# Performance work log

Measured on AMD Instinct MI355X. Metric: run time of the kernel, lower is better.

Reference implementation:

```python
import jax, jax.numpy as jnp
import numpy as np

H = 12        # num_attention_heads
D = 768       # hidden_size
DH = D // H   # attention_size per head (64)
B, S = 1, 4096


def setup_inputs() -> dict:
    key = jax.random.key(0)
    ks = jax.random.split(key, 10)
    scale = 0.02
    x = jax.random.normal(ks[0], (B, S, D), dtype=jnp.float32)
    # per-head QKV weights stacked: [H, D, DH]
    wq = jax.random.normal(ks[1], (H, D, DH), dtype=jnp.float32) * scale
    wk = jax.random.normal(ks[2], (H, D, DH), dtype=jnp.float32) * scale
    wv = jax.random.normal(ks[3], (H, D, DH), dtype=jnp.float32) * scale
    bq = jax.random.normal(ks[4], (H, DH), dtype=jnp.float32) * scale
    bk = jax.random.normal(ks[5], (H, DH), dtype=jnp.float32) * scale
    bv = jax.random.normal(ks[6], (H, DH), dtype=jnp.float32) * scale
    wo = jax.random.normal(ks[7], (D, D), dtype=jnp.float32) * scale
    bo = jax.random.normal(ks[8], (D,), dtype=jnp.float32) * scale
    return {"x": x, "wq": wq, "bq": bq, "wk": wk, "bk": bk,
            "wv": wv, "bv": bv, "wo": wo, "bo": bo}


def reference(x, wq, bq, wk, bk, wv, bv, wo, bo):
    # per-head linear projections: [B,S,D] x [H,D,DH] -> [B,H,S,DH]
    q = jnp.einsum('bsd,hde->bhse', x, wq) + bq[None, :, None, :]
    k = jnp.einsum('bsd,hde->bhse', x, wk) + bk[None, :, None, :]
    v = jnp.einsum('bsd,hde->bhse', x, wv) + bv[None, :, None, :]
    # scaled dot-product attention, full NxN probs as in original
    scores = jnp.einsum('bhse,bhte->bhst', q, k) / jnp.sqrt(jnp.float32(DH))
    probs = jax.nn.softmax(scores, axis=-1)          # [B,H,S,S]
    ctx = jnp.einsum('bhst,bhte->bhse', probs, v)    # [B,H,S,DH]
    # concat heads along feature dim (head order = original ModuleList order)
    ctx = jnp.transpose(ctx, (0, 2, 1, 3)).reshape(B, S, H * DH)
    out = ctx @ wo + bo                               # output projection
    return out
```

## Files before the change

### kernel.cpp

```cpp
#include <hip/hip_runtime.h>


using frag8 = __attribute__((ext_vector_type(8))) short;
using facc4 = __attribute__((ext_vector_type(4))) float;
using uint4v = __attribute__((ext_vector_type(4))) unsigned int;

#define LOG2E 1.4426950408889634f
#define THR_LOG2 11.5415603f
#define SWZ16(r, b) ((b) ^ (((r) & 7) << 4))

#if defined(__has_builtin)
#  if __has_builtin(__builtin_amdgcn_exp2f)
#    define EXP2(x) __builtin_amdgcn_exp2f(x)
#  else
#    define EXP2(x) exp2f(x)
#  endif
#else
#  define EXP2(x) exp2f(x)
#endif

__device__ __forceinline__ unsigned short f2bf(float f) {
  unsigned int u = __builtin_bit_cast(unsigned int, f);
  u = (u + 0x7FFFu + ((u >> 16) & 1u)) >> 16;
  return (unsigned short)u;
}
__device__ __forceinline__ float bf2f(unsigned short s) {
  unsigned int u = ((unsigned int)s) << 16;
  return __builtin_bit_cast(float, u);
}
__device__ __forceinline__ unsigned cvt_pk_bf16(float lo, float hi) {
  unsigned r;
  asm("v_cvt_pk_bf16_f32 %0, %1, %2" : "=v"(r) : "v"(lo), "v"(hi));
  return r;
}

__device__ __forceinline__ facc4 mfma_bf16(frag8 a, frag8 b, facc4 c) {
  return __builtin_amdgcn_mfma_f32_16x16x32_bf16(a, b, c, 0, 0, 0);
}

__device__ __forceinline__ void gld_lds16(const void* g, void* l) {
  auto gp = (const __attribute__((address_space(1))) unsigned int*)g;
  auto lp = (__attribute__((address_space(3))) unsigned int*)l;
  __builtin_amdgcn_global_load_lds(gp, lp, 16, 0, 0);
}

__global__ __launch_bounds__(256) void k_cvt_x(const float* __restrict__ in,
                                               unsigned short* __restrict__ out) {
  int i = (blockIdx.x * 256 + threadIdx.x) * 8;
  float4 a = *(const float4*)(in + i);
  float4 b = *(const float4*)(in + i + 4);
  frag8 r;
  r[0] = (short)f2bf(a.x); r[1] = (short)f2bf(a.y);
  r[2] = (short)f2bf(a.z); r[3] = (short)f2bf(a.w);
  r[4] = (short)f2bf(b.x); r[5] = (short)f2bf(b.y);
  r[6] = (short)f2bf(b.z); r[7] = (short)f2bf(b.w);
  *(frag8*)(out + i) = r;
}

__global__ __launch_bounds__(256) void k_prep_w(
    const float* __restrict__ wq, const float* __restrict__ wk,
    const float* __restrict__ wv, const float* __restrict__ wo,
    unsigned short* __restrict__ wqT, unsigned short* __restrict__ wkT,
    unsigned short* __restrict__ wvT, unsigned short* __restrict__ woT) {
  __shared__ unsigned short tile[64][65];
  const int bx = blockIdx.x;
  const float* src; unsigned short* dst;
  int ld_src, ld_dst, r0, c0;
  if (bx < 432) {
    int p = bx / 144, rem = bx % 144;
    int h = rem / 12, dt = rem % 12;
    src = (p == 0 ? wq : (p == 1 ? wk : wv)) + (size_t)h * 768 * 64;
    dst = (p == 0 ? wqT : (p == 1 ? wkT : wvT)) + (size_t)h * 64 * 768;
    ld_src = 64; ld_dst = 768; r0 = dt * 64; c0 = 0;
  } else {
    int t = bx - 432;
    src = wo; dst = woT;
    ld_src = 768; ld_dst = 768;
    r0 = (t / 12) * 64; c0 = (t % 12) * 64;
  }
  const int tid = threadIdx.x;
  const int lr = tid >> 2, lc0 = (tid & 3) * 16;
#pragma unroll
  for (int i = 0; i < 16; ++i)
    tile[lr][lc0 + i] = f2bf(src[(size_t)(r0 + lr) * ld_src + c0 + lc0 + i]);
  __syncthreads();
  const int oc = tid >> 2;
#pragma unroll
  for (int i = 0; i < 16; ++i)
    dst[(size_t)(c0 + oc) * ld_dst + r0 + lc0 + i] = tile[lc0 + i][oc];
}

__global__ __launch_bounds__(256) void k_qkv(
    const unsigned short* __restrict__ xb, const unsigned short* __restrict__ wT,
    const float* __restrict__ bq, const float* __restrict__ bk,
    const float* __restrict__ bv,
    unsigned short* __restrict__ qo, unsigned short* __restrict__ ko,
    unsigned short* __restrict__ vTo) {
  __shared__ __align__(16) unsigned short As[128 * 64];
  __shared__ __align__(16) unsigned short Bs[64 * 64];
  const int sb = blockIdx.x, ph = blockIdx.y;
  const int p = ph / 12, h = ph % 12;
  const int s0 = sb * 128;
  const int tid = threadIdx.x;
  const int w = tid >> 6, l = tid & 63;
  const int lg = l >> 4, li = l & 15;
  const int wm = w >> 1, wn = w & 1;
  const unsigned short* wTb = wT + (size_t)ph * 64 * 768;

  facc4 acc[4][2];
#pragma unroll
  for (int i = 0; i < 4; ++i)
#pragma unroll
    for (int j = 0; j < 2; ++j) acc[i][j] = (facc4){0.f, 0.f, 0.f, 0.f};

  const int rA = tid >> 3;
  const int cbp = (tid & 7) * 16;

  for (int k0 = 0; k0 < 768; k0 += 64) {
#pragma unroll
    for (int i = 0; i < 4; ++i) {
      int r = i * 32 + rA;
      gld_lds16((const char*)(xb + (size_t)(s0 + r) * 768 + k0) + SWZ16(r, cbp),
                (char*)As + i * 4096 + w * 1024);
    }
#pragma unroll
    for (int i = 0; i < 2; ++i) {
      int r = i * 32 + rA;
      gld_lds16((const char*)(wTb + (size_t)r * 768 + k0) + SWZ16(r, cbp),
                (char*)Bs + i * 4096 + w * 1024);
    }
    __syncthreads();
#pragma unroll
    for (int kk = 0; kk < 2; ++kk) {
      const int cbl = kk * 64 + lg * 16;
      frag8 a[4], b[2];
#pragma unroll
      for (int mf = 0; mf < 4; ++mf) {
        int r = wm * 64 + mf * 16 + li;
        a[mf] = *(const frag8*)((const char*)As + r * 128 + SWZ16(r, cbl));
      }
#pragma unroll
      for (int nf = 0; nf < 2; ++nf) {
        int r = wn * 32 + nf * 16 + li;
        b[nf] = *(const frag8*)((const char*)Bs + r * 128 + SWZ16(r, cbl));
      }
#pragma unroll
      for (int mf = 0; mf < 4; ++mf)
#pragma unroll
        for (int nf = 0; nf < 2; ++nf)
          acc[mf][nf] = mfma_bf16(a[mf], b[nf], acc[mf][nf]);
    }
    __syncthreads();
  }

  const float* bias = (p == 0 ? bq : (p == 1 ? bk : bv)) + h * 64;
  const float scale = (p == 0) ? 0.125f * LOG2E : 1.0f;
  float bvv[2];
#pragma unroll
  for (int nf = 0; nf < 2; ++nf) bvv[nf] = bias[wn * 32 + nf * 16 + li];
#pragma unroll
  for (int mf = 0; mf < 4; ++mf)
#pragma unroll
    for (int nf = 0; nf < 2; ++nf) {
      int e = wn * 32 + nf * 16 + li;
#pragma unroll
      for (int j = 0; j < 4; ++j) {
        int s = s0 + wm * 64 + mf * 16 + lg * 4 + j;
        unsigned short bf = f2bf((acc[mf][nf][j] + bvv[nf]) * scale);
        if (p == 0)      qo[((size_t)h * 4096 + s) * 64 + e] = bf;
        else if (p == 1) ko[((size_t)h * 4096 + s) * 64 + e] = bf;
        else             vTo[((size_t)h * 64 + e) * 4096 + s] = bf;
      }
    }
}

__global__ __launch_bounds__(512) void k_attn(
    const unsigned short* __restrict__ q, const unsigned short* __restrict__ k,
    const unsigned short* __restrict__ vT,
    unsigned short* __restrict__ oP, float* __restrict__ mlP) {
  __shared__ __align__(16) char Kb[2][8192];
  __shared__ __align__(16) char Vb[2][8192];
  const int bid = blockIdx.x;
  const int part = blockIdx.y;
  const int h = bid >> 5, qb = bid & 31;
  const int s0 = qb * 128;
  const int tid = threadIdx.x;
  const int w = tid >> 6, l = tid & 63;
  const int lg = l >> 4, li = l & 15;
  const unsigned short* Kh = k + (size_t)h * 4096 * 64;
  const unsigned short* Vh = vT + (size_t)h * 64 * 4096;

  const int rS = tid >> 3;
  const int bS = (tid & 7) * 16;
  const int sbS = SWZ16(rS, bS);

  const unsigned short* qrow = q + ((size_t)h * 4096 + s0 + w * 16 + li) * 64;
  frag8 qf0 = *(const frag8*)(qrow + lg * 8);
  frag8 qf1 = *(const frag8*)(qrow + 32 + lg * 8);

  frag8 onesf;
#pragma unroll
  for (int i = 0; i < 8; ++i) onesf[i] = (short)0x3F80;

  const int a_ = li >> 2, b_ = li & 3;
  const int r_base = 8 * a_ + b_;
  int kOff[4][2], vOff[4][2];
#pragma unroll
  for (int cn = 0; cn < 4; ++cn) {
    int r = r_base + 4 * ((cn & 1) ^ (a_ & 1)) + 32 * (cn >> 1);
    kOff[cn][0] = r * 128 + SWZ16(r, lg * 16);
    kOff[cn][1] = r * 128 + SWZ16(r, 64 + lg * 16);
  }
#pragma unroll
  for (int nf = 0; nf < 4; ++nf) {
    int rv = nf * 16 + li;
    vOff[nf][0] = rv * 128 + SWZ16(rv, lg * 16);
    vOff[nf][1] = rv * 128 + SWZ16(rv, 64 + lg * 16);
  }
  const char* KbC = (const char*)Kb;
  const char* VbC = (const char*)Vb;

  float m = -1e30f;
  facc4 acc[4];
  facc4 accl = (facc4){0.f, 0.f, 0.f, 0.f};
#pragma unroll
  for (int nf = 0; nf < 4; ++nf) acc[nf] = (facc4){0.f, 0.f, 0.f, 0.f};

  const int kb0 = part * 2048;

  gld_lds16((const char*)(Kh + (size_t)(kb0 + rS) * 64) + sbS, (char*)Kb + w * 1024);
  gld_lds16((const char*)(Vh + (size_t)rS * 4096 + kb0) + sbS, (char*)Vb + w * 1024);
  const char* KgN = (const char*)(Kh + (size_t)(kb0 + 64 + rS) * 64) + sbS;
  const char* VgN = (const char*)(Vh + (size_t)rS * 4096 + kb0 + 64) + sbS;
  __syncthreads();

#define ATTN_STEP(BUFB, KT)                                                   \
  {                                                                           \
    if ((KT) < 31) {                                                          \
      gld_lds16(KgN, (char*)Kb + ((BUFB) ^ 8192) + w * 1024);                 \
      gld_lds16(VgN, (char*)Vb + ((BUFB) ^ 8192) + w * 1024);                 \
      KgN += 8192; VgN += 128;                                                \
    }                                                                         \
    facc4 sf[4];                                                              \
    __builtin_amdgcn_s_setprio(1);                                            \
    _Pragma("unroll")                                                         \
    for (int cn = 0; cn < 4; ++cn) {                                          \
      frag8 a0 = *(const frag8*)(KbC + (BUFB) + kOff[cn][0]);                 \
      frag8 a1 = *(const frag8*)(KbC + (BUFB) + kOff[cn][1]);                 \
      facc4 s = (facc4){0.f, 0.f, 0.f, 0.f};                                  \
      s = mfma_bf16(a0, qf0, s);                                              \
      s = mfma_bf16(a1, qf1, s);                                              \
      sf[cn] = s;                                                             \
    }                                                                         \
    __builtin_amdgcn_s_setprio(0);                                            \
    if (lg & 1) {                                                             \
      facc4 t_ = sf[0]; sf[0] = sf[1]; sf[1] = t_;                            \
      t_ = sf[2]; sf[2] = sf[3]; sf[3] = t_;                                  \
    }                                                                         \
    float t = fmaxf(fmaxf(sf[0][0], sf[0][1]), sf[0][2]);                     \
    t = fmaxf(fmaxf(t, sf[0][3]), sf[1][0]);                                  \
    t = fmaxf(fmaxf(t, sf[1][1]), sf[1][2]);                                  \
    t = fmaxf(fmaxf(t, sf[1][3]), sf[2][0]);                                  \
    t = fmaxf(fmaxf(t, sf[2][1]), sf[2][2]);                                  \
    t = fmaxf(fmaxf(t, sf[2][3]), sf[3][0]);                                  \
    t = fmaxf(fmaxf(t, sf[3][1]), sf[3][2]);                                  \
    float tmax = fmaxf(t, sf[3][3]);                                          \
    tmax = fmaxf(tmax, __shfl_xor(tmax, 16));                                 \
    tmax = fmaxf(tmax, __shfl_xor(tmax, 32));                                 \
    if (__any(tmax > m + THR_LOG2)) {                                         \
      float mn = fmaxf(m, tmax);                                              \
      float corr = EXP2(m - mn);                                              \
      m = mn;                                                                 \
      _Pragma("unroll")                                                       \
      for (int j = 0; j < 4; ++j) {                                           \
        float cj = __shfl(corr, (l & 48) | (4 * lg + j));                     \
        accl[j] *= cj;                                                        \
        _Pragma("unroll")                                                     \
        for (int nf = 0; nf < 4; ++nf) acc[nf][j] *= cj;                      \
      }                                                                       \
    }                                                                         \
    float pv[4][4];                                                           \
    _Pragma("unroll")                                                         \
    for (int cn = 0; cn < 4; ++cn)                                            \
      _Pragma("unroll")                                                       \
      for (int j = 0; j < 4; ++j)                                             \
        pv[cn][j] = EXP2(sf[cn][j] - m);                                      \
    uint4v u0, u1;                                                            \
    u0[0] = cvt_pk_bf16(pv[0][0], pv[0][1]);                                  \
    u0[1] = cvt_pk_bf16(pv[0][2], pv[0][3]);                                  \
    u0[2] = cvt_pk_bf16(pv[1][0], pv[1][1]);                                  \
    u0[3] = cvt_pk_bf16(pv[1][2], pv[1][3]);                                  \
    u1[0] = cvt_pk_bf16(pv[2][0], pv[2][1]);                                  \
    u1[1] = cvt_pk_bf16(pv[2][2], pv[2][3]);                                  \
    u1[2] = cvt_pk_bf16(pv[3][0], pv[3][1]);                                  \
    u1[3] = cvt_pk_bf16(pv[3][2], pv[3][3]);                                  \
    frag8 pa0 = __builtin_bit_cast(frag8, u0);                                \
    frag8 pa1 = __builtin_bit_cast(frag8, u1);                                \
    __builtin_amdgcn_s_setprio(1);                                            \
    accl = mfma_bf16(pa0, onesf, accl);                                       \
    accl = mfma_bf16(pa1, onesf, accl);                                       \
    _Pragma("unroll")                                                         \
    for (int nf = 0; nf < 4; ++nf) {                                          \
      frag8 vb0 = *(const frag8*)(VbC + (BUFB) + vOff[nf][0]);                \
      frag8 vb1 = *(const frag8*)(VbC + (BUFB) + vOff[nf][1]);                \
      acc[nf] = mfma_bf16(pa0, vb0, acc[nf]);                                 \
      acc[nf] = mfma_bf16(pa1, vb1, acc[nf]);                                 \
    }                                                                         \
    __builtin_amdgcn_s_setprio(0);                                            \
    __syncthreads();                                                          \
  }

  for (int t2 = 0; t2 < 16; ++t2) {
    ATTN_STEP(0, 2 * t2)
    ATTN_STEP(8192, 2 * t2 + 1)
  }
#undef ATTN_STEP

  const size_t base = ((size_t)(part * 12 + h) * 4096 + s0 + w * 16);
#pragma unroll
  for (int nf = 0; nf < 4; ++nf)
#pragma unroll
    for (int j = 0; j < 4; ++j)
      oP[(base + lg * 4 + j) * 64 + nf * 16 + li] = f2bf(acc[nf][j] / accl[j]);
  if (lg == 0)
    mlP[(base + li) * 2 + 0] = m;
  if (li == 0) {
#pragma unroll
    for (int j = 0; j < 4; ++j)
      mlP[(base + lg * 4 + j) * 2 + 1] = accl[j];
  }
}

__global__ __launch_bounds__(256) void k_combine(
    const unsigned short* __restrict__ oP, const float* __restrict__ mlP,
    unsigned short* __restrict__ ctx) {
  const int tid = threadIdx.x;
  const int rg = blockIdx.x * 4 + (tid >> 6);
  const int e = tid & 63;
  const int h = rg >> 12, s = rg & 4095;
  const size_t r0 = (size_t)h * 4096 + s;
  const size_t r1 = (size_t)(12 + h) * 4096 + s;
  float m0 = mlP[r0 * 2], l0 = mlP[r0 * 2 + 1];
  float m1 = mlP[r1 * 2], l1 = mlP[r1 * 2 + 1];
  float M = fmaxf(m0, m1);
  float w0 = l0 * EXP2(m0 - M);
  float w1 = l1 * EXP2(m1 - M);
  float inv = 1.f / (w0 + w1);
  float o = (w0 * bf2f(oP[r0 * 64 + e]) + w1 * bf2f(oP[r1 * 64 + e])) * inv;
  ctx[(size_t)s * 768 + h * 64 + e] = f2bf(o);
}

__global__ __launch_bounds__(256) void k_proj(
    const unsigned short* __restrict__ ctx, const unsigned short* __restrict__ woT,
    const float* __restrict__ bo, float* __restrict__ out) {
  __shared__ __align__(16) unsigned short As[64 * 64];
  __shared__ __align__(16) unsigned short Bs[64 * 64];
  const int s0 = blockIdx.x * 64, j0 = blockIdx.y * 64;
  const int tid = threadIdx.x;
  const int w = tid >> 6, l = tid & 63;
  const int lg = l >> 4, li = l & 15;
  const int wm = w >> 1, wn = w & 1;
  facc4 acc[2][2];
#pragma unroll
  for (int i = 0; i < 2; ++i)
#pragma unroll
    for (int j = 0; j < 2; ++j) acc[i][j] = (facc4){0.f, 0.f, 0.f, 0.f};

  const int rA = tid >> 3;
  const int cbp = (tid & 7) * 16;

  for (int k0 = 0; k0 < 768; k0 += 64) {
#pragma unroll
    for (int i = 0; i < 2; ++i) {
      int r = i * 32 + rA;
      gld_lds16((const char*)(ctx + (size_t)(s0 + r) * 768 + k0) + SWZ16(r, cbp),
                (char*)As + i * 4096 + w * 1024);
      gld_lds16((const char*)(woT + (size_t)(j0 + r) * 768 + k0) + SWZ16(r, cbp),
                (char*)Bs + i * 4096 + w * 1024);
    }
    __syncthreads();
#pragma unroll
    for (int kk = 0; kk < 2; ++kk) {
      const int cbl = kk * 64 + lg * 16;
      frag8 a[2], b[2];
#pragma unroll
      for (int mf = 0; mf < 2; ++mf) {
        int r = wm * 32 + mf * 16 + li;
        a[mf] = *(const frag8*)((const char*)As + r * 128 + SWZ16(r, cbl));
      }
#pragma unroll
      for (int nf = 0; nf < 2; ++nf) {
        int r = wn * 32 + nf * 16 + li;
        b[nf] = *(const frag8*)((const char*)Bs + r * 128 + SWZ16(r, cbl));
      }
#pragma unroll
      for (int mf = 0; mf < 2; ++mf)
#pragma unroll
        for (int nf = 0; nf < 2; ++nf)
          acc[mf][nf] = mfma_bf16(a[mf], b[nf], acc[mf][nf]);
    }
    __syncthreads();
  }
#pragma unroll
  for (int nf = 0; nf < 2; ++nf) {
    int jc = j0 + wn * 32 + nf * 16 + li;
    float bb = bo[jc];
#pragma unroll
    for (int mf = 0; mf < 2; ++mf)
#pragma unroll
      for (int j = 0; j < 4; ++j) {
        int s = s0 + wm * 32 + mf * 16 + lg * 4 + j;
        out[(size_t)s * 768 + jc] = acc[mf][nf][j] + bb;
      }
  }
}

extern "C" void kernel_launch(void* const* d_in, const int* in_sizes, int n_in,
                              void* d_out, int out_size, void* d_ws, size_t ws_size,
                              hipStream_t stream) {
  const float* x  = (const float*)d_in[0];
  const float* wq = (const float*)d_in[1];
  const float* bq = (const float*)d_in[2];
  const float* wk = (const float*)d_in[3];
  const float* bk = (const float*)d_in[4];
  const float* wv = (const float*)d_in[5];
  const float* bv = (const float*)d_in[6];
  const float* wo = (const float*)d_in[7];
  const float* bo = (const float*)d_in[8];
  float* out = (float*)d_out;

  char* ws = (char*)d_ws;
  unsigned short* xb  = (unsigned short*)(ws);
  unsigned short* wT  = (unsigned short*)(ws + 6291456);
  unsigned short* woT = (unsigned short*)(ws + 9830400);
  unsigned short* qd  = (unsigned short*)(ws + 11010048);
  unsigned short* kd  = (unsigned short*)(ws + 17301504);
  unsigned short* vTd = (unsigned short*)(ws + 23592960);
  unsigned short* ctx = (unsigned short*)(ws + 29884416);
  unsigned short* oP  = (unsigned short*)(ws + 36175872);
  float*          mlP = (float*)(ws + 48758784);

  k_cvt_x<<<1536, 256, 0, stream>>>(x, xb);
  k_prep_w<<<576, 256, 0, stream>>>(wq, wk, wv, wo,
                                    wT, wT + 589824, wT + 1179648, woT);
  k_qkv<<<dim3(32, 36), 256, 0, stream>>>(xb, wT, bq, bk, bv, qd, kd, vTd);
  k_attn<<<dim3(384, 2), 512, 0, stream>>>(qd, kd, vTd, oP, mlP);
  k_combine<<<12288, 256, 0, stream>>>(oP, mlP, ctx);
  k_proj<<<dim3(64, 12), 256, 0, stream>>>(ctx, woT, bo, out);
}
```

Measured before the change: 137.1 us.

## Triple-buffer attention K/V loads and widen QKV GEMM tile to 128 columns

The attention kernel moves from double to triple buffering of K/V tiles in LDS. It replaces __syncthreads with an explicit s_waitcnt vmcnt(2) plus s_barrier, so the next tile's loads stay in flight across the barrier. The QKV projection kernel now computes 128x128 tiles covering two heads per block, halving the grid and reusing each loaded x tile across twice as many output columns. The costs are higher LDS use per block in both kernels and more accumulator registers in QKV, which may reduce occupancy.

```diff
diff --git a/kernel.cpp b/kernel.cpp
--- a/kernel.cpp
+++ b/kernel.cpp
@@ -97,21 +97,19 @@
     unsigned short* __restrict__ qo, unsigned short* __restrict__ ko,
     unsigned short* __restrict__ vTo) {
   __shared__ __align__(16) unsigned short As[128 * 64];
-  __shared__ __align__(16) unsigned short Bs[64 * 64];
-  const int sb = blockIdx.x, ph = blockIdx.y;
-  const int p = ph / 12, h = ph % 12;
-  const int s0 = sb * 128;
+  __shared__ __align__(16) unsigned short Bs[128 * 64];
+  const int sb = blockIdx.x, nb = blockIdx.y;
+  const int s0 = sb * 128, c0 = nb * 128;
   const int tid = threadIdx.x;
   const int w = tid >> 6, l = tid & 63;
   const int lg = l >> 4, li = l & 15;
   const int wm = w >> 1, wn = w & 1;
-  const unsigned short* wTb = wT + (size_t)ph * 64 * 768;
-
-  facc4 acc[4][2];
+
+  facc4 acc[4][4];
 #pragma unroll
   for (int i = 0; i < 4; ++i)
 #pragma unroll
-    for (int j = 0; j < 2; ++j) acc[i][j] = (facc4){0.f, 0.f, 0.f, 0.f};
+    for (int j = 0; j < 4; ++j) acc[i][j] = (facc4){0.f, 0.f, 0.f, 0.f};
 
   const int rA = tid >> 3;
   const int cbp = (tid & 7) * 16;
@@ -122,64 +120,60 @@
       int r = i * 32 + rA;
       gld_lds16((const char*)(xb + (size_t)(s0 + r) * 768 + k0) + SWZ16(r, cbp),
                 (char*)As + i * 4096 + w * 1024);
-    }
-#pragma unroll
-    for (int i = 0; i < 2; ++i) {
-      int r = i * 32 + rA;
-      gld_lds16((const char*)(wTb + (size_t)r * 768 + k0) + SWZ16(r, cbp),
+      gld_lds16((const char*)(wT + (size_t)(c0 + r) * 768 + k0) + SWZ16(r, cbp),
                 (char*)Bs + i * 4096 + w * 1024);
     }
     __syncthreads();
 #pragma unroll
     for (int kk = 0; kk < 2; ++kk) {
       const int cbl = kk * 64 + lg * 16;
-      frag8 a[4], b[2];
+      frag8 a[4], b[4];
 #pragma unroll
       for (int mf = 0; mf < 4; ++mf) {
         int r = wm * 64 + mf * 16 + li;
         a[mf] = *(const frag8*)((const char*)As + r * 128 + SWZ16(r, cbl));
       }
 #pragma unroll
-      for (int nf = 0; nf < 2; ++nf) {
-        int r = wn * 32 + nf * 16 + li;
+      for (int nf = 0; nf < 4; ++nf) {
+        int r = wn * 64 + nf * 16 + li;
         b[nf] = *(const frag8*)((const char*)Bs + r * 128 + SWZ16(r, cbl));
       }
 #pragma unroll
       for (int mf = 0; mf < 4; ++mf)
 #pragma unroll
-        for (int nf = 0; nf < 2; ++nf)
+        for (int nf = 0; nf < 4; ++nf)
           acc[mf][nf] = mfma_bf16(a[mf], b[nf], acc[mf][nf]);
     }
     __syncthreads();
   }
 
+  const int ph = nb * 2 + wn;
+  const int p = ph / 12, h = ph % 12;
   const float* bias = (p == 0 ? bq : (p == 1 ? bk : bv)) + h * 64;
   const float scale = (p == 0) ? 0.125f * LOG2E : 1.0f;
-  float bvv[2];
-#pragma unroll
-  for (int nf = 0; nf < 2; ++nf) bvv[nf] = bias[wn * 32 + nf * 16 + li];
-#pragma unroll
-  for (int mf = 0; mf < 4; ++mf)
-#pragma unroll
-    for (int nf = 0; nf < 2; ++nf) {
-      int e = wn * 32 + nf * 16 + li;
+#pragma unroll
+  for (int nf = 0; nf < 4; ++nf) {
+    int e = nf * 16 + li;
+    float bvv = bias[e];
+#pragma unroll
+    for (int mf = 0; mf < 4; ++mf)
 #pragma unroll
       for (int j = 0; j < 4; ++j) {
         int s = s0 + wm * 64 + mf * 16 + lg * 4 + j;
-        unsigned short bf = f2bf((acc[mf][nf][j] + bvv[nf]) * scale);
+        unsigned short bf = f2bf((acc[mf][nf][j] + bvv) * scale);
         if (p == 0)      qo[((size_t)h * 4096 + s) * 64 + e] = bf;
         else if (p == 1) ko[((size_t)h * 4096 + s) * 64 + e] = bf;
         else             vTo[((size_t)h * 64 + e) * 4096 + s] = bf;
       }
-    }
+  }
 }
 
 __global__ __launch_bounds__(512) void k_attn(
     const unsigned short* __restrict__ q, const unsigned short* __restrict__ k,
     const unsigned short* __restrict__ vT,
     unsigned short* __restrict__ oP, float* __restrict__ mlP) {
-  __shared__ __align__(16) char Kb[2][8192];
-  __shared__ __align__(16) char Vb[2][8192];
+  __shared__ __align__(16) char Kb[3][8192];
+  __shared__ __align__(16) char Vb[3][8192];
   const int bid = blockIdx.x;
   const int part = blockIdx.y;
   const int h = bid >> 5, qb = bid & 31;
@@ -228,25 +222,32 @@
 
   const int kb0 = part * 2048;
 
-  gld_lds16((const char*)(Kh + (size_t)(kb0 + rS) * 64) + sbS, (char*)Kb + w * 1024);
-  gld_lds16((const char*)(Vh + (size_t)rS * 4096 + kb0) + sbS, (char*)Vb + w * 1024);
-  const char* KgN = (const char*)(Kh + (size_t)(kb0 + 64 + rS) * 64) + sbS;
-  const char* VgN = (const char*)(Vh + (size_t)rS * 4096 + kb0 + 64) + sbS;
-  __syncthreads();
-
-#define ATTN_STEP(BUFB, KT)                                                   \
+  gld_lds16((const char*)(Kh + (size_t)(kb0 + rS) * 64) + sbS,
+            (char*)Kb + w * 1024);
+  gld_lds16((const char*)(Vh + (size_t)rS * 4096 + kb0) + sbS,
+            (char*)Vb + w * 1024);
+  gld_lds16((const char*)(Kh + (size_t)(kb0 + 64 + rS) * 64) + sbS,
+            (char*)Kb + 8192 + w * 1024);
+  gld_lds16((const char*)(Vh + (size_t)rS * 4096 + kb0 + 64) + sbS,
+            (char*)Vb + 8192 + w * 1024);
+  const char* KgN = (const char*)(Kh + (size_t)(kb0 + 128 + rS) * 64) + sbS;
+  const char* VgN = (const char*)(Vh + (size_t)rS * 4096 + kb0 + 128) + sbS;
+  asm volatile("s_waitcnt vmcnt(2)" ::: "memory");
+  __builtin_amdgcn_s_barrier();
+
+#define ATTN_STEP(CURB, NXTB, DO_ISSUE, DO_SYNC, VMSTR)                       \
   {                                                                           \
-    if ((KT) < 31) {                                                          \
-      gld_lds16(KgN, (char*)Kb + ((BUFB) ^ 8192) + w * 1024);                 \
-      gld_lds16(VgN, (char*)Vb + ((BUFB) ^ 8192) + w * 1024);                 \
+    if (DO_ISSUE) {                                                           \
+      gld_lds16(KgN, (char*)Kb + (NXTB) + w * 1024);                          \
+      gld_lds16(VgN, (char*)Vb + (NXTB) + w * 1024);                          \
       KgN += 8192; VgN += 128;                                                \
     }                                                                         \
     facc4 sf[4];                                                              \
     __builtin_amdgcn_s_setprio(1);                                            \
     _Pragma("unroll")                                                         \
     for (int cn = 0; cn < 4; ++cn) {                                          \
-      frag8 a0 = *(const frag8*)(KbC + (BUFB) + kOff[cn][0]);                 \
-      frag8 a1 = *(const frag8*)(KbC + (BUFB) + kOff[cn][1]);                 \
+      frag8 a0 = *(const frag8*)(KbC + (CURB) + kOff[cn][0]);                 \
+      frag8 a1 = *(const frag8*)(KbC + (CURB) + kOff[cn][1]);                 \
       facc4 s = (facc4){0.f, 0.f, 0.f, 0.f};                                  \
       s = mfma_bf16(a0, qf0, s);                                              \
       s = mfma_bf16(a1, qf1, s);                                              \
@@ -301,19 +302,25 @@
     accl = mfma_bf16(pa1, onesf, accl);                                       \
     _Pragma("unroll")                                                         \
     for (int nf = 0; nf < 4; ++nf) {                                          \
-      frag8 vb0 = *(const frag8*)(VbC + (BUFB) + vOff[nf][0]);                \
-      frag8 vb1 = *(const frag8*)(VbC + (BUFB) + vOff[nf][1]);                \
+      frag8 vb0 = *(const frag8*)(VbC + (CURB) + vOff[nf][0]);                \
+      frag8 vb1 = *(const frag8*)(VbC + (CURB) + vOff[nf][1]);                \
       acc[nf] = mfma_bf16(pa0, vb0, acc[nf]);                                 \
       acc[nf] = mfma_bf16(pa1, vb1, acc[nf]);                                 \
     }                                                                         \
     __builtin_amdgcn_s_setprio(0);                                            \
-    __syncthreads();                                                          \
-  }
-
-  for (int t2 = 0; t2 < 16; ++t2) {
-    ATTN_STEP(0, 2 * t2)
-    ATTN_STEP(8192, 2 * t2 + 1)
-  }
+    if (DO_SYNC) {                                                            \
+      asm volatile("s_waitcnt " VMSTR ::: "memory");                          \
+      __builtin_amdgcn_s_barrier();                                           \
+    }                                                                         \
+  }
+
+  for (int t3 = 0; t3 < 10; ++t3) {
+    ATTN_STEP(0,     16384, true, true, "vmcnt(2)")
+    ATTN_STEP(8192,  0,     true, true, "vmcnt(2)")
+    ATTN_STEP(16384, 8192,  true, true, "vmcnt(2)")
+  }
+  ATTN_STEP(0,    0, false, true,  "vmcnt(0)")
+  ATTN_STEP(8192, 0, false, false, "")
 #undef ATTN_STEP
 
   const size_t base = ((size_t)(part * 12 + h) * 4096 + s0 + w * 16);
@@ -443,7 +450,7 @@
   k_cvt_x<<<1536, 256, 0, stream>>>(x, xb);
   k_prep_w<<<576, 256, 0, stream>>>(wq, wk, wv, wo,
                                     wT, wT + 589824, wT + 1179648, woT);
-  k_qkv<<<dim3(32, 36), 256, 0, stream>>>(xb, wT, bq, bk, bv, qd, kd, vTd);
+  k_qkv<<<dim3(32, 18), 256, 0, stream>>>(xb, wT, bq, bk, bv, qd, kd, vTd);
   k_attn<<<dim3(384, 2), 512, 0, stream>>>(qd, kd, vTd, oP, mlP);
   k_combine<<<12288, 256, 0, stream>>>(oP, mlP, ctx);
   k_proj<<<dim3(64, 12), 256, 0, stream>>>(ctx, woT, bo, out);
```

Measured after the change: 151.5 us. 1.1x slower.

## Switch attention kernel to 32x32x16 MFMA with 32 query rows per wave

Applied to the files above, without the earlier changes.

Rewrites the flash-attention inner loop to use the 32x32x16 bf16 MFMA instead of 16x16x32. Each wave now owns 32 query rows, so the block shrinks from 8 to 4 waves while still covering 128 queries, and the K/V tile loads are split into two gld_lds calls per thread. Fewer, larger MFMAs and a longer row of scores per lane are meant to cut instruction count and LDS fragment reads per FLOP. The cost is more accumulator registers and fewer waves per block to hide latency.

```diff
diff --git a/kernel.cpp b/kernel.cpp
--- a/kernel.cpp
+++ b/kernel.cpp
@@ -1,8 +1,9 @@
 #include <hip/hip_runtime.h>
 
 
-using frag8 = __attribute__((ext_vector_type(8))) short;
-using facc4 = __attribute__((ext_vector_type(4))) float;
+using frag8  = __attribute__((ext_vector_type(8))) short;
+using facc4  = __attribute__((ext_vector_type(4))) float;
+using facc16 = __attribute__((ext_vector_type(16))) float;
 using uint4v = __attribute__((ext_vector_type(4))) unsigned int;
 
 #define LOG2E 1.4426950408889634f
@@ -36,6 +37,9 @@
 
 __device__ __forceinline__ facc4 mfma_bf16(frag8 a, frag8 b, facc4 c) {
   return __builtin_amdgcn_mfma_f32_16x16x32_bf16(a, b, c, 0, 0, 0);
+}
+__device__ __forceinline__ facc16 mfma32(frag8 a, frag8 b, facc16 c) {
+  return __builtin_amdgcn_mfma_f32_32x32x16_bf16(a, b, c, 0, 0, 0);
 }
 
 __device__ __forceinline__ void gld_lds16(const void* g, void* l) {
@@ -174,7 +178,7 @@
     }
 }
 
-__global__ __launch_bounds__(512) void k_attn(
+__global__ __launch_bounds__(256) void k_attn(
     const unsigned short* __restrict__ q, const unsigned short* __restrict__ k,
     const unsigned short* __restrict__ vT,
     unsigned short* __restrict__ oP, float* __restrict__ mlP) {
@@ -186,125 +190,148 @@
   const int s0 = qb * 128;
   const int tid = threadIdx.x;
   const int w = tid >> 6, l = tid & 63;
-  const int lg = l >> 4, li = l & 15;
+  const int q5 = l & 31, hi = l >> 5;
   const unsigned short* Kh = k + (size_t)h * 4096 * 64;
   const unsigned short* Vh = vT + (size_t)h * 64 * 4096;
 
   const int rS = tid >> 3;
   const int bS = (tid & 7) * 16;
-  const int sbS = SWZ16(rS, bS);
-
-  const unsigned short* qrow = q + ((size_t)h * 4096 + s0 + w * 16 + li) * 64;
-  frag8 qf0 = *(const frag8*)(qrow + lg * 8);
-  frag8 qf1 = *(const frag8*)(qrow + 32 + lg * 8);
+  const int sb0 = SWZ16(rS, bS);
+  const int sb1 = SWZ16(rS + 32, bS);
+
+  const unsigned short* qrow = q + ((size_t)h * 4096 + s0 + w * 32 + q5) * 64;
+  frag8 qf[4];
+#pragma unroll
+  for (int st = 0; st < 4; ++st)
+    qf[st] = *(const frag8*)(qrow + st * 16 + 8 * hi);
 
   frag8 onesf;
 #pragma unroll
   for (int i = 0; i < 8; ++i) onesf[i] = (short)0x3F80;
 
-  const int a_ = li >> 2, b_ = li & 3;
-  const int r_base = 8 * a_ + b_;
-  int kOff[4][2], vOff[4][2];
-#pragma unroll
-  for (int cn = 0; cn < 4; ++cn) {
-    int r = r_base + 4 * ((cn & 1) ^ (a_ & 1)) + 32 * (cn >> 1);
-    kOff[cn][0] = r * 128 + SWZ16(r, lg * 16);
-    kOff[cn][1] = r * 128 + SWZ16(r, 64 + lg * 16);
-  }
-#pragma unroll
-  for (int nf = 0; nf < 4; ++nf) {
-    int rv = nf * 16 + li;
-    vOff[nf][0] = rv * 128 + SWZ16(rv, lg * 16);
-    vOff[nf][1] = rv * 128 + SWZ16(rv, 64 + lg * 16);
-  }
+  const int key0 = (q5 & ~12) | ((q5 & 4) << 1) | ((q5 & 8) >> 1);
+  int kOff[2][4], vOff[2][4];
+#pragma unroll
+  for (int kh = 0; kh < 2; ++kh)
+#pragma unroll
+    for (int st = 0; st < 4; ++st) {
+      int kr = kh * 32 + key0;
+      kOff[kh][st] = kr * 128 + SWZ16(kr, st * 32 + hi * 16);
+    }
+#pragma unroll
+  for (int eh = 0; eh < 2; ++eh)
+#pragma unroll
+    for (int ks = 0; ks < 4; ++ks) {
+      int rv = eh * 32 + q5;
+      vOff[eh][ks] = rv * 128 + SWZ16(rv, ks * 32 + hi * 16);
+    }
   const char* KbC = (const char*)Kb;
   const char* VbC = (const char*)Vb;
 
   float m = -1e30f;
-  facc4 acc[4];
-  facc4 accl = (facc4){0.f, 0.f, 0.f, 0.f};
-#pragma unroll
-  for (int nf = 0; nf < 4; ++nf) acc[nf] = (facc4){0.f, 0.f, 0.f, 0.f};
+  facc16 acc0, acc1, accl;
+#pragma unroll
+  for (int r = 0; r < 16; ++r) { acc0[r] = 0.f; acc1[r] = 0.f; accl[r] = 0.f; }
 
   const int kb0 = part * 2048;
 
-  gld_lds16((const char*)(Kh + (size_t)(kb0 + rS) * 64) + sbS, (char*)Kb + w * 1024);
-  gld_lds16((const char*)(Vh + (size_t)rS * 4096 + kb0) + sbS, (char*)Vb + w * 1024);
-  const char* KgN = (const char*)(Kh + (size_t)(kb0 + 64 + rS) * 64) + sbS;
-  const char* VgN = (const char*)(Vh + (size_t)rS * 4096 + kb0 + 64) + sbS;
+  gld_lds16((const char*)(Kh + (size_t)(kb0 + rS) * 64) + sb0,
+            (char*)Kb + w * 1024);
+  gld_lds16((const char*)(Kh + (size_t)(kb0 + 32 + rS) * 64) + sb1,
+            (char*)Kb + 4096 + w * 1024);
+  gld_lds16((const char*)(Vh + (size_t)rS * 4096 + kb0) + sb0,
+            (char*)Vb + w * 1024);
+  gld_lds16((const char*)(Vh + (size_t)(rS + 32) * 4096 + kb0) + sb1,
+            (char*)Vb + 4096 + w * 1024);
+  const char* Kg0 = (const char*)(Kh + (size_t)(kb0 + 64 + rS) * 64) + sb0;
+  const char* Kg1 = (const char*)(Kh + (size_t)(kb0 + 96 + rS) * 64) + sb1;
+  const char* Vg0 = (const char*)(Vh + (size_t)rS * 4096 + kb0 + 64) + sb0;
+  const char* Vg1 = (const char*)(Vh + (size_t)(rS + 32) * 4096 + kb0 + 64) + sb1;
   __syncthreads();
 
 #define ATTN_STEP(BUFB, KT)                                                   \
   {                                                                           \
     if ((KT) < 31) {                                                          \
-      gld_lds16(KgN, (char*)Kb + ((BUFB) ^ 8192) + w * 1024);                 \
-      gld_lds16(VgN, (char*)Vb + ((BUFB) ^ 8192) + w * 1024);                 \
-      KgN += 8192; VgN += 128;                                                \
-    }                                                                         \
-    facc4 sf[4];                                                              \
+      gld_lds16(Kg0, (char*)Kb + ((BUFB) ^ 8192) + w * 1024);                 \
+      gld_lds16(Kg1, (char*)Kb + ((BUFB) ^ 8192) + 4096 + w * 1024);          \
+      gld_lds16(Vg0, (char*)Vb + ((BUFB) ^ 8192) + w * 1024);                 \
+      gld_lds16(Vg1, (char*)Vb + ((BUFB) ^ 8192) + 4096 + w * 1024);          \
+      Kg0 += 8192; Kg1 += 8192; Vg0 += 128; Vg1 += 128;                       \
+    }                                                                         \
+    facc16 sf0, sf1;                                                          \
+    _Pragma("unroll")                                                         \
+    for (int r = 0; r < 16; ++r) { sf0[r] = 0.f; sf1[r] = 0.f; }              \
     __builtin_amdgcn_s_setprio(1);                                            \
     _Pragma("unroll")                                                         \
-    for (int cn = 0; cn < 4; ++cn) {                                          \
-      frag8 a0 = *(const frag8*)(KbC + (BUFB) + kOff[cn][0]);                 \
-      frag8 a1 = *(const frag8*)(KbC + (BUFB) + kOff[cn][1]);                 \
-      facc4 s = (facc4){0.f, 0.f, 0.f, 0.f};                                  \
-      s = mfma_bf16(a0, qf0, s);                                              \
-      s = mfma_bf16(a1, qf1, s);                                              \
-      sf[cn] = s;                                                             \
+    for (int st = 0; st < 4; ++st) {                                          \
+      frag8 a0 = *(const frag8*)(KbC + (BUFB) + kOff[0][st]);                 \
+      sf0 = mfma32(a0, qf[st], sf0);                                          \
+    }                                                                         \
+    _Pragma("unroll")                                                         \
+    for (int st = 0; st < 4; ++st) {                                          \
+      frag8 a1 = *(const frag8*)(KbC + (BUFB) + kOff[1][st]);                 \
+      sf1 = mfma32(a1, qf[st], sf1);                                          \
     }                                                                         \
     __builtin_amdgcn_s_setprio(0);                                            \
-    if (lg & 1) {                                                             \
-      facc4 t_ = sf[0]; sf[0] = sf[1]; sf[1] = t_;                            \
-      t_ = sf[2]; sf[2] = sf[3]; sf[3] = t_;                                  \
-    }                                                                         \
-    float t = fmaxf(fmaxf(sf[0][0], sf[0][1]), sf[0][2]);                     \
-    t = fmaxf(fmaxf(t, sf[0][3]), sf[1][0]);                                  \
-    t = fmaxf(fmaxf(t, sf[1][1]), sf[1][2]);                                  \
-    t = fmaxf(fmaxf(t, sf[1][3]), sf[2][0]);                                  \
-    t = fmaxf(fmaxf(t, sf[2][1]), sf[2][2]);                                  \
-    t = fmaxf(fmaxf(t, sf[2][3]), sf[3][0]);                                  \
-    t = fmaxf(fmaxf(t, sf[3][1]), sf[3][2]);                                  \
-    float tmax = fmaxf(t, sf[3][3]);                                          \
-    tmax = fmaxf(tmax, __shfl_xor(tmax, 16));                                 \
+    float ta = fmaxf(fmaxf(sf0[0], sf0[1]), fmaxf(sf0[2], sf0[3]));           \
+    float tb = fmaxf(fmaxf(sf0[4], sf0[5]), fmaxf(sf0[6], sf0[7]));           \
+    float tc = fmaxf(fmaxf(sf0[8], sf0[9]), fmaxf(sf0[10], sf0[11]));         \
+    float td = fmaxf(fmaxf(sf0[12], sf0[13]), fmaxf(sf0[14], sf0[15]));       \
+    float te = fmaxf(fmaxf(sf1[0], sf1[1]), fmaxf(sf1[2], sf1[3]));           \
+    float tf = fmaxf(fmaxf(sf1[4], sf1[5]), fmaxf(sf1[6], sf1[7]));           \
+    float tg = fmaxf(fmaxf(sf1[8], sf1[9]), fmaxf(sf1[10], sf1[11]));         \
+    float th = fmaxf(fmaxf(sf1[12], sf1[13]), fmaxf(sf1[14], sf1[15]));       \
+    float tmax = fmaxf(fmaxf(fmaxf(ta, tb), fmaxf(tc, td)),                   \
+                       fmaxf(fmaxf(te, tf), fmaxf(tg, th)));                  \
     tmax = fmaxf(tmax, __shfl_xor(tmax, 32));                                 \
     if (__any(tmax > m + THR_LOG2)) {                                         \
       float mn = fmaxf(m, tmax);                                              \
       float corr = EXP2(m - mn);                                              \
       m = mn;                                                                 \
       _Pragma("unroll")                                                       \
-      for (int j = 0; j < 4; ++j) {                                           \
-        float cj = __shfl(corr, (l & 48) | (4 * lg + j));                     \
-        accl[j] *= cj;                                                        \
-        _Pragma("unroll")                                                     \
-        for (int nf = 0; nf < 4; ++nf) acc[nf][j] *= cj;                      \
+      for (int r = 0; r < 16; ++r) {                                          \
+        float cj = __shfl(corr, (r & 3) + 8 * (r >> 2) + 4 * hi);             \
+        accl[r] *= cj; acc0[r] *= cj; acc1[r] *= cj;                          \
       }                                                                       \
     }                                                                         \
-    float pv[4][4];                                                           \
+    uint4v u00, u01, u10, u11;                                                \
     _Pragma("unroll")                                                         \
-    for (int cn = 0; cn < 4; ++cn)                                            \
-      _Pragma("unroll")                                                       \
-      for (int j = 0; j < 4; ++j)                                             \
-        pv[cn][j] = EXP2(sf[cn][j] - m);                                      \
-    uint4v u0, u1;                                                            \
-    u0[0] = cvt_pk_bf16(pv[0][0], pv[0][1]);                                  \
-    u0[1] = cvt_pk_bf16(pv[0][2], pv[0][3]);                                  \
-    u0[2] = cvt_pk_bf16(pv[1][0], pv[1][1]);                                  \
-    u0[3] = cvt_pk_bf16(pv[1][2], pv[1][3]);                                  \
-    u1[0] = cvt_pk_bf16(pv[2][0], pv[2][1]);                                  \
-    u1[1] = cvt_pk_bf16(pv[2][2], pv[2][3]);                                  \
-    u1[2] = cvt_pk_bf16(pv[3][0], pv[3][1]);                                  \
-    u1[3] = cvt_pk_bf16(pv[3][2], pv[3][3]);                                  \
-    frag8 pa0 = __builtin_bit_cast(frag8, u0);                                \
-    frag8 pa1 = __builtin_bit_cast(frag8, u1);                                \
+    for (int p2 = 0; p2 < 4; ++p2) {                                          \
+      u00[p2] = cvt_pk_bf16(EXP2(sf0[2 * p2] - m), EXP2(sf0[2 * p2 + 1] - m));\
+      u01[p2] = cvt_pk_bf16(EXP2(sf0[8 + 2 * p2] - m),                        \
+                            EXP2(sf0[8 + 2 * p2 + 1] - m));                   \
+      u10[p2] = cvt_pk_bf16(EXP2(sf1[2 * p2] - m), EXP2(sf1[2 * p2 + 1] - m));\
+      u11[p2] = cvt_pk_bf16(EXP2(sf1[8 + 2 * p2] - m),                        \
+                            EXP2(sf1[8 + 2 * p2 + 1] - m));                   \
+    }                                                                         \
+    frag8 pa00 = __builtin_bit_cast(frag8, u00);                              \
+    frag8 pa01 = __builtin_bit_cast(frag8, u01);                              \
+    frag8 pa10 = __builtin_bit_cast(frag8, u10);                              \
+    frag8 pa11 = __builtin_bit_cast(frag8, u11);                              \
     __builtin_amdgcn_s_setprio(1);                                            \
-    accl = mfma_bf16(pa0, onesf, accl);                                       \
-    accl = mfma_bf16(pa1, onesf, accl);                                       \
-    _Pragma("unroll")                                                         \
-    for (int nf = 0; nf < 4; ++nf) {                                          \
-      frag8 vb0 = *(const frag8*)(VbC + (BUFB) + vOff[nf][0]);                \
-      frag8 vb1 = *(const frag8*)(VbC + (BUFB) + vOff[nf][1]);                \
-      acc[nf] = mfma_bf16(pa0, vb0, acc[nf]);                                 \
-      acc[nf] = mfma_bf16(pa1, vb1, acc[nf]);                                 \
+    accl = mfma32(pa00, onesf, accl);                                         \
+    accl = mfma32(pa01, onesf, accl);                                         \
+    accl = mfma32(pa10, onesf, accl);                                         \
+    accl = mfma32(pa11, onesf, accl);                                         \
+    {                                                                         \
+      frag8 vb0 = *(const frag8*)(VbC + (BUFB) + vOff[0][0]);                 \
+      frag8 vb1 = *(const frag8*)(VbC + (BUFB) + vOff[0][1]);                 \
+      frag8 vb2 = *(const frag8*)(VbC + (BUFB) + vOff[0][2]);                 \
+      frag8 vb3 = *(const frag8*)(VbC + (BUFB) + vOff[0][3]);                 \
+      acc0 = mfma32(pa00, vb0, acc0);                                         \
+      acc0 = mfma32(pa01, vb1, acc0);                                         \
+      acc0 = mfma32(pa10, vb2, acc0);                                         \
+      acc0 = mfma32(pa11, vb3, acc0);                                         \
+    }                                                                         \
+    {                                                                         \
+      frag8 vb0 = *(const frag8*)(VbC + (BUFB) + vOff[1][0]);                 \
+      frag8 vb1 = *(const frag8*)(VbC + (BUFB) + vOff[1][1]);                 \
+      frag8 vb2 = *(const frag8*)(VbC + (BUFB) + vOff[1][2]);                 \
+      frag8 vb3 = *(const frag8*)(VbC + (BUFB) + vOff[1][3]);                 \
+      acc1 = mfma32(pa00, vb0, acc1);                                         \
+      acc1 = mfma32(pa01, vb1, acc1);                                         \
+      acc1 = mfma32(pa10, vb2, acc1);                                         \
+      acc1 = mfma32(pa11, vb3, acc1);                                         \
     }                                                                         \
     __builtin_amdgcn_s_setprio(0);                                            \
     __syncthreads();                                                          \
@@ -316,18 +343,22 @@
   }
 #undef ATTN_STEP
 
-  const size_t base = ((size_t)(part * 12 + h) * 4096 + s0 + w * 16);
-#pragma unroll
-  for (int nf = 0; nf < 4; ++nf)
-#pragma unroll
-    for (int j = 0; j < 4; ++j)
-      oP[(base + lg * 4 + j) * 64 + nf * 16 + li] = f2bf(acc[nf][j] / accl[j]);
-  if (lg == 0)
-    mlP[(base + li) * 2 + 0] = m;
-  if (li == 0) {
-#pragma unroll
-    for (int j = 0; j < 4; ++j)
-      mlP[(base + lg * 4 + j) * 2 + 1] = accl[j];
+  const size_t base = ((size_t)(part * 12 + h) * 4096 + s0 + w * 32);
+#pragma unroll
+  for (int r = 0; r < 16; ++r) {
+    int row = (r & 3) + 8 * (r >> 2) + 4 * hi;
+    float inv = 1.f / accl[r];
+    oP[(base + row) * 64 + q5]      = f2bf(acc0[r] * inv);
+    oP[(base + row) * 64 + 32 + q5] = f2bf(acc1[r] * inv);
+  }
+  if (hi == 0)
+    mlP[(base + q5) * 2 + 0] = m;
+  if (q5 == 0) {
+#pragma unroll
+    for (int r = 0; r < 16; ++r) {
+      int row = (r & 3) + 8 * (r >> 2) + 4 * hi;
+      mlP[(base + row) * 2 + 1] = accl[r];
+    }
   }
 }
 
@@ -444,7 +475,7 @@
   k_prep_w<<<576, 256, 0, stream>>>(wq, wk, wv, wo,
                                     wT, wT + 589824, wT + 1179648, woT);
   k_qkv<<<dim3(32, 36), 256, 0, stream>>>(xb, wT, bq, bk, bv, qd, kd, vTd);
-  k_attn<<<dim3(384, 2), 512, 0, stream>>>(qd, kd, vTd, oP, mlP);
+  k_attn<<<dim3(384, 2), 256, 0, stream>>>(qd, kd, vTd, oP, mlP);
   k_combine<<<12288, 256, 0, stream>>>(oP, mlP, ctx);
   k_proj<<<dim3(64, 12), 256, 0, stream>>>(ctx, woT, bo, out);
 }
```

After: 143.5 us. +4.7%, slower.
